# Kernel tuning notes

Hardware: AMD Instinct MI355X
Metric: run time of the kernel (lower is better)

## Reference

```python
import jax, jax.numpy as jnp
import numpy as np

HEADS, D_K = 8, 64   # dim=512 -> d_k = dim//heads = 64; with dim_head=64 the rearrange collapses to [B,H,N,d_k]
EPS = 1e-5


def _per_head_layernorm(t, g, b):
    # t: [B,H,N,D]; g,b: [H,D] (independent LayerNorm per head, biased variance like torch)
    mu = t.mean(-1, keepdims=True)
    var = ((t - mu) ** 2).mean(-1, keepdims=True)
    return (t - mu) * jax.lax.rsqrt(var + EPS) * g[None, :, None, :] + b[None, :, None, :]


def setup_inputs() -> dict:
    key = jax.random.key(0)
    k0, k1, k2, k3, k4, k5 = jax.random.split(key, 6)
    B, N, DIM = 4, 2048, 512
    inner = HEADS * D_K  # = DIM here
    x = jax.random.normal(k0, (B, N, DIM), jnp.float32)
    W_qkv = jax.random.normal(k1, (DIM, 3 * inner), jnp.float32) * (DIM ** -0.5)  # xavier-ish, no bias
    g_q = 1.0 + 0.1 * jax.random.normal(k2, (HEADS, D_K), jnp.float32)
    b_q = 0.1 * jax.random.normal(k3, (HEADS, D_K), jnp.float32)
    g_k = 1.0 + 0.1 * jax.random.normal(k4, (HEADS, D_K), jnp.float32)
    b_k = 0.1 * jax.random.normal(k5, (HEADS, D_K), jnp.float32)
    return {"x": x, "W_qkv": W_qkv, "g_q": g_q, "b_q": b_q, "g_k": g_k, "b_k": b_k}


def reference(x, W_qkv, g_q, b_q, g_k, b_k):
    B, N, _ = x.shape
    qkv = x @ W_qkv                              # [B,N,3*H*D]
    q, k, v = jnp.split(qkv, 3, axis=-1)

    def split_heads(t):
        return t.reshape(B, N, HEADS, D_K).transpose(0, 2, 1, 3)  # [B,H,N,D]

    q, k, v = map(split_heads, (q, k, v))
    q = _per_head_layernorm(q, g_q, b_q)
    k = _per_head_layernorm(k, g_k, b_k)
    # un-normalized linear attention: scale by 1/sqrt(d_k) then by 1/seq_len (no softmax)
    dots = jnp.einsum('bhnd,bhmd->bhnm', q, k) * (D_K ** -0.5)
    p_attn = dots / N
    out = jnp.einsum('bhnm,bhmd->bhnd', p_attn, v)  # [B,H,N,D]
    return out.transpose(0, 2, 1, 3).reshape(B, N, HEADS * D_K)
```

## Files before the change

kernel.cpp:

```cpp
#include <hip/hip_runtime.h>
#include <hip/hip_bf16.h>
#include <stdint.h>

using bf16   = __bf16;
using bf16x4 = __attribute__((ext_vector_type(4))) __bf16;
using bf16x8 = __attribute__((ext_vector_type(8))) __bf16;
using f32x4  = __attribute__((ext_vector_type(4))) float;

static constexpr int BATCH = 4, SEQ = 2048, DIM = 512, HEADS = 8, DK = 64;
static constexpr int M    = BATCH * SEQ;
static constexpr int NQKV = 3 * DIM;

#define GLD16(src, dst)                                                        \
    __builtin_amdgcn_global_load_lds(                                          \
        (const __attribute__((address_space(1))) void*)(src),                  \
        (__attribute__((address_space(3))) void*)(dst), 16, 0, 0)

__global__ __launch_bounds__(256) void k_prep(const float* __restrict__ x,
                                              const float* __restrict__ w,
                                              bf16* __restrict__ xbf,
                                              bf16* __restrict__ wt,
                                              float* __restrict__ S)
{
    const int bid = blockIdx.x;
    const int t   = threadIdx.x;
    const int XB  = (M * DIM) / (256 * 4);
    const int WB  = (DIM / 32) * (NQKV / 32);

    if (bid < XB) {
        const int i = (bid * 256 + t) * 4;
        float4 v = *(const float4*)(x + i);
        bf16x4 o = { (bf16)v.x, (bf16)v.y, (bf16)v.z, (bf16)v.w };
        *(bf16x4*)(xbf + i) = o;
    } else if (bid < XB + WB) {
        const int wb = bid - XB;
        const int rt = wb / 48, ct = wb - rt * 48;
        __shared__ float tile[32][33];
        const int r = t >> 5, c = t & 31;
        #pragma unroll
        for (int i = 0; i < 4; ++i)
            tile[r + i * 8][c] = w[(rt * 32 + r + i * 8) * NQKV + ct * 32 + c];
        __syncthreads();
        #pragma unroll
        for (int i = 0; i < 4; ++i)
            wt[(ct * 32 + r + i * 8) * DIM + rt * 32 + c] = (bf16)tile[c][r + i * 8];
    } else {
        const int sb = bid - XB - WB;
        const int i  = (sb * 256 + t) * 4;
        *(f32x4*)(S + i) = (f32x4){0.f, 0.f, 0.f, 0.f};
    }
}

__global__ __launch_bounds__(384) void k_gemm(const bf16* __restrict__ xbf,
                                              const bf16* __restrict__ Wt,
                                              const float* __restrict__ gq,
                                              const float* __restrict__ bq,
                                              const float* __restrict__ gk,
                                              const float* __restrict__ bk,
                                              bf16* __restrict__ qn,
                                              float* __restrict__ S)
{
    __shared__ union {
        struct { bf16 A[2][128 * 64]; bf16 B[2][192 * 64]; } g;
        struct { bf16 q[2][64][72]; bf16 kst[64 * 128]; bf16 vst[64 * 128]; } e;
    } u;

    const int t    = threadIdx.x;
    const int lane = t & 63, wave = t >> 6;
    const int wm   = wave & 1, ws = wave >> 1;
    const int orig = blockIdx.x;
    const int wg   = (orig & 7) * 64 + (orig >> 3);
    const int mt   = wg >> 3, h = wg & 7;
    const int m0   = mt * 128;

    const int l15 = lane & 15, l4 = lane >> 4;
    const int rl  = lane >> 3, cl = (lane & 7) ^ rl;

    auto stage = [&](int buf, int k0) {
        for (int c = wave; c < 40; c += 6) {
            if (c < 16) {
                const int r = c * 8 + rl;
                GLD16(xbf + (m0 + r) * 512 + k0 + cl * 8, u.g.A[buf] + c * 512);
            } else {
                const int ch  = c - 16;
                const int sec = ch >> 3;
                const int r   = (ch & 7) * 8 + rl;
                GLD16(Wt + ((sec * 512 + h * 64 + r) * 512 + k0 + cl * 8),
                      u.g.B[buf] + ch * 512);
            }
        }
    };

    f32x4 acc[4][4] = {};

    stage(0, 0);
    __syncthreads();
    int cur = 0;
    for (int it = 0; it < 8; ++it) {
        if (it < 7) stage(cur ^ 1, (it + 1) * 64);
        #pragma unroll
        for (int kh = 0; kh < 2; ++kh) {
            bf16x8 af[4], bfv[4];
            const int rc = kh * 4 + l4;
            #pragma unroll
            for (int mf = 0; mf < 4; ++mf) {
                const int row = wm * 64 + mf * 16 + l15;
                af[mf] = *(const bf16x8*)(u.g.A[cur] + row * 64 + ((rc ^ (row & 7)) * 8));
            }
            #pragma unroll
            for (int nf = 0; nf < 4; ++nf) {
                const int row = ws * 64 + nf * 16 + l15;
                bfv[nf] = *(const bf16x8*)(u.g.B[cur] + row * 64 + ((rc ^ (row & 7)) * 8));
            }
            #pragma unroll
            for (int mf = 0; mf < 4; ++mf)
                #pragma unroll
                for (int nf = 0; nf < 4; ++nf)
                    acc[mf][nf] = __builtin_amdgcn_mfma_f32_16x16x32_bf16(
                        af[mf], bfv[nf], acc[mf][nf], 0, 0, 0);
        }
        __syncthreads();
        cur ^= 1;
    }

    const int b  = m0 >> 11;
    const int bh = b * 8 + h;
    const int nwbase = (m0 & 2047) + wm * 64;

    if (ws < 2) {
        const float* gp = (ws == 0 ? gq : gk) + h * 64;
        const float* bp = (ws == 0 ? bq : bk) + h * 64;
        float gv[4], bv[4];
        #pragma unroll
        for (int nf = 0; nf < 4; ++nf) {
            gv[nf] = gp[nf * 16 + l15];
            bv[nf] = bp[nf * 16 + l15];
        }
        #pragma unroll
        for (int mf = 0; mf < 4; ++mf) {
            float mu[4], rs[4];
            #pragma unroll
            for (int r = 0; r < 4; ++r) {
                float s = 0.f, s2 = 0.f;
                #pragma unroll
                for (int nf = 0; nf < 4; ++nf) {
                    const float xv = acc[mf][nf][r];
                    s += xv; s2 += xv * xv;
                }
                s  += __shfl_xor(s, 1);  s  += __shfl_xor(s, 2);
                s  += __shfl_xor(s, 4);  s  += __shfl_xor(s, 8);
                s2 += __shfl_xor(s2, 1); s2 += __shfl_xor(s2, 2);
                s2 += __shfl_xor(s2, 4); s2 += __shfl_xor(s2, 8);
                mu[r] = s * (1.f / 64.f);
                rs[r] = rsqrtf(s2 * (1.f / 64.f) - mu[r] * mu[r] + 1e-5f);
            }
            #pragma unroll
            for (int nf = 0; nf < 4; ++nf) {
                bf16x4 pk;
                #pragma unroll
                for (int r = 0; r < 4; ++r)
                    pk[r] = (bf16)((acc[mf][nf][r] - mu[r]) * rs[r] * gv[nf] + bv[nf]);
                if (ws == 0) {
                    *(bf16x4*)(&u.e.q[wm][nf * 16 + l15][mf * 16 + l4 * 4]) = pk;
                } else {
                    const int d = nf * 16 + l15;
                    const int c = wm * 8 + mf * 2 + (l4 >> 1);
                    *(bf16x4*)(u.e.kst + d * 128 + ((c ^ (d & 7)) * 8) + (l4 & 1) * 4) = pk;
                }
            }
        }
    } else {
        #pragma unroll
        for (int mf = 0; mf < 4; ++mf)
            #pragma unroll
            for (int nf = 0; nf < 4; ++nf) {
                bf16x4 pk;
                #pragma unroll
                for (int r = 0; r < 4; ++r) pk[r] = (bf16)acc[mf][nf][r];
                const int d = nf * 16 + l15;
                const int c = wm * 8 + mf * 2 + (l4 >> 1);
                *(bf16x4*)(u.e.vst + d * 128 + ((c ^ (d & 7)) * 8) + (l4 & 1) * 4) = pk;
            }
    }

    if (ws == 0) {
        bf16* dst = qn + ((long)bh * SEQ + nwbase) * 64;
        const int nq = lane & 15, dq2 = lane >> 4;
        #pragma unroll
        for (int j = 0; j < 4; ++j) {
            const int d0 = (j * 4 + dq2) * 4;
            bf16x4 a0 = *(const bf16x4*)(&u.e.q[wm][d0 + 0][nq * 4]);
            bf16x4 a1 = *(const bf16x4*)(&u.e.q[wm][d0 + 1][nq * 4]);
            bf16x4 a2 = *(const bf16x4*)(&u.e.q[wm][d0 + 2][nq * 4]);
            bf16x4 a3 = *(const bf16x4*)(&u.e.q[wm][d0 + 3][nq * 4]);
            #pragma unroll
            for (int c = 0; c < 4; ++c) {
                bf16x4 o = { a0[c], a1[c], a2[c], a3[c] };
                *(bf16x4*)(dst + (nq * 4 + c) * 64 + d0) = o;
            }
        }
    }

    __syncthreads();

    if (ws == 2) {
        f32x4 sac[4][4] = {};
        #pragma unroll
        for (int kk = 0; kk < 2; ++kk) {
            const int ksi = wm * 2 + kk;
            const int c   = ksi * 4 + l4;
            bf16x8 av[4], bk8[4];
            #pragma unroll
            for (int i = 0; i < 4; ++i) {
                const int dp = i * 16 + l15;
                av[i] = *(const bf16x8*)(u.e.vst + dp * 128 + ((c ^ (dp & 7)) * 8));
            }
            #pragma unroll
            for (int j = 0; j < 4; ++j) {
                const int dd = j * 16 + l15;
                bk8[j] = *(const bf16x8*)(u.e.kst + dd * 128 + ((c ^ (dd & 7)) * 8));
            }
            #pragma unroll
            for (int i = 0; i < 4; ++i)
                #pragma unroll
                for (int j = 0; j < 4; ++j)
                    sac[i][j] = __builtin_amdgcn_mfma_f32_16x16x32_bf16(
                        av[i], bk8[j], sac[i][j], 0, 0, 0);
        }
        float* Sb = S + bh * 4096;
        #pragma unroll
        for (int i = 0; i < 4; ++i)
            #pragma unroll
            for (int j = 0; j < 4; ++j)
                #pragma unroll
                for (int r = 0; r < 4; ++r) {
                    const int dp = i * 16 + l4 * 4 + r;
                    const int dd = j * 16 + l15;
                    atomicAdd(Sb + dp * 64 + dd, sac[i][j][r]);
                }
    }
}

__global__ __launch_bounds__(256) void k_out(const bf16* __restrict__ qn,
                                             const float* __restrict__ S,
                                             float* __restrict__ out)
{
    const int bid = blockIdx.x;
    const int bh = bid >> 4, nt4 = bid & 15;
    const int b = bh >> 3, h = bh & 7;
    const int t = threadIdx.x, lane = t & 63, wave = t >> 6;
    const int l15 = lane & 15, l4 = lane >> 4;
    const float* Sb = S + bh * 4096;
    const float scale = 1.f / 16384.f;

    bf16x8 bfr[2][4];
    #pragma unroll
    for (int kh = 0; kh < 2; ++kh)
        #pragma unroll
        for (int cf = 0; cf < 4; ++cf) {
            const float* p = Sb + (cf * 16 + l15) * 64 + kh * 32 + l4 * 8;
            float4 lo = *(const float4*)(p);
            float4 hi = *(const float4*)(p + 4);
            bf16x8 f;
            f[0] = (bf16)(lo.x * scale); f[1] = (bf16)(lo.y * scale);
            f[2] = (bf16)(lo.z * scale); f[3] = (bf16)(lo.w * scale);
            f[4] = (bf16)(hi.x * scale); f[5] = (bf16)(hi.y * scale);
            f[6] = (bf16)(hi.z * scale); f[7] = (bf16)(hi.w * scale);
            bfr[kh][cf] = f;
        }

    const bf16* qb = qn + (long)bh * SEQ * 64;
    const int nbase = nt4 * 128 + wave * 32;

    #pragma unroll
    for (int mf = 0; mf < 2; ++mf) {
        bf16x8 a0 = *(const bf16x8*)(qb + (nbase + mf * 16 + l15) * 64 +      l4 * 8);
        bf16x8 a1 = *(const bf16x8*)(qb + (nbase + mf * 16 + l15) * 64 + 32 + l4 * 8);
        f32x4 acc[4] = {};
        #pragma unroll
        for (int cf = 0; cf < 4; ++cf) {
            acc[cf] = __builtin_amdgcn_mfma_f32_16x16x32_bf16(a0, bfr[0][cf], acc[cf], 0, 0, 0);
            acc[cf] = __builtin_amdgcn_mfma_f32_16x16x32_bf16(a1, bfr[1][cf], acc[cf], 0, 0, 0);
        }
        #pragma unroll
        for (int cf = 0; cf < 4; ++cf)
            #pragma unroll
            for (int r = 0; r < 4; ++r) {
                const int n = nbase + mf * 16 + l4 * 4 + r;
                out[((long)b * SEQ + n) * 512 + h * 64 + cf * 16 + l15] = acc[cf][r];
            }
    }
}

extern "C" void kernel_launch(void* const* d_in, const int* in_sizes, int n_in,
                              void* d_out, int out_size, void* d_ws, size_t ws_size,
                              hipStream_t stream)
{
    const float* x  = (const float*)d_in[0];
    const float* w  = (const float*)d_in[1];
    const float* gq = (const float*)d_in[2];
    const float* bq = (const float*)d_in[3];
    const float* gk = (const float*)d_in[4];
    const float* bk = (const float*)d_in[5];
    float* out = (float*)d_out;

    char* ws = (char*)d_ws;
    bf16*  xbf = (bf16*)(ws);
    bf16*  wt  = (bf16*)(ws + 8388608);
    bf16*  qn  = (bf16*)(ws + 9961472);
    float* S   = (float*)(ws + 18350080);

    hipLaunchKernelGGL(k_prep, dim3(4096 + 768 + 128), dim3(256), 0, stream,
                       x, w, xbf, wt, S);
    hipLaunchKernelGGL(k_gemm, dim3(512), dim3(384), 0, stream,
                       xbf, wt, gq, bq, gk, bk, qn, S);
    hipLaunchKernelGGL(k_out,  dim3(512), dim3(256), 0, stream, qn, S, out);
}
```

Baseline: 129.3 us.

## Triple-buffer GEMM K-loop with 32-wide slices and explicit vmcnt waits

```diff
diff --git a/kernel.cpp b/kernel.cpp
--- a/kernel.cpp
+++ b/kernel.cpp
@@ -15,6 +15,9 @@
     __builtin_amdgcn_global_load_lds(                                          \
         (const __attribute__((address_space(1))) void*)(src),                  \
         (__attribute__((address_space(3))) void*)(dst), 16, 0, 0)
+
+#define WAITVM(N)  asm volatile("s_waitcnt vmcnt(" #N ")" ::: "memory")
+#define WAITLGKM0  asm volatile("s_waitcnt lgkmcnt(0)" ::: "memory")
 
 __global__ __launch_bounds__(256) void k_prep(const float* __restrict__ x,
                                               const float* __restrict__ w,
@@ -61,7 +64,7 @@
                                               float* __restrict__ S)
 {
     __shared__ union {
-        struct { bf16 A[2][128 * 64]; bf16 B[2][192 * 64]; } g;
+        struct { bf16 A[3][128 * 32]; bf16 B[3][192 * 32]; } g;
         struct { bf16 q[2][64][72]; bf16 kst[64 * 128]; bf16 vst[64 * 128]; } e;
     } u;
 
@@ -74,54 +77,68 @@
     const int m0   = mt * 128;
 
     const int l15 = lane & 15, l4 = lane >> 4;
-    const int rl  = lane >> 3, cl = (lane & 7) ^ rl;
-
-    auto stage = [&](int buf, int k0) {
-        for (int c = wave; c < 40; c += 6) {
-            if (c < 16) {
-                const int r = c * 8 + rl;
-                GLD16(xbf + (m0 + r) * 512 + k0 + cl * 8, u.g.A[buf] + c * 512);
+    const int r4l = lane >> 2, c4 = lane & 3;
+
+    auto stage = [&](int sl, int k0) {
+        for (int c = wave; c < 20; c += 6) {
+            if (c < 8) {
+                const int r = c * 16 + r4l;
+                GLD16(xbf + (m0 + r) * 512 + k0 + ((c4 ^ (r & 3)) * 8),
+                      u.g.A[sl] + c * 512);
             } else {
-                const int ch  = c - 16;
-                const int sec = ch >> 3;
-                const int r   = (ch & 7) * 8 + rl;
-                GLD16(Wt + ((sec * 512 + h * 64 + r) * 512 + k0 + cl * 8),
-                      u.g.B[buf] + ch * 512);
+                const int rb  = (c - 8) * 16 + r4l;
+                const int sec = rb >> 6, rin = rb & 63;
+                GLD16(Wt + ((sec * 512 + h * 64 + rin) * 512 + k0 + ((c4 ^ (rb & 3)) * 8)),
+                      u.g.B[sl] + (c - 8) * 512);
             }
         }
     };
 
     f32x4 acc[4][4] = {};
 
+    auto compute = [&](int sl) {
+        bf16x8 af[4], bfv[4];
+        #pragma unroll
+        for (int mf = 0; mf < 4; ++mf) {
+            const int row = wm * 64 + mf * 16 + l15;
+            af[mf] = *(const bf16x8*)(u.g.A[sl] + row * 32 + ((l4 ^ (row & 3)) * 8));
+        }
+        #pragma unroll
+        for (int nf = 0; nf < 4; ++nf) {
+            const int row = ws * 64 + nf * 16 + l15;
+            bfv[nf] = *(const bf16x8*)(u.g.B[sl] + row * 32 + ((l4 ^ (row & 3)) * 8));
+        }
+        #pragma unroll
+        for (int mf = 0; mf < 4; ++mf)
+            #pragma unroll
+            for (int nf = 0; nf < 4; ++nf)
+                acc[mf][nf] = __builtin_amdgcn_mfma_f32_16x16x32_bf16(
+                    af[mf], bfv[nf], acc[mf][nf], 0, 0, 0);
+    };
+
     stage(0, 0);
-    __syncthreads();
-    int cur = 0;
-    for (int it = 0; it < 8; ++it) {
-        if (it < 7) stage(cur ^ 1, (it + 1) * 64);
-        #pragma unroll
-        for (int kh = 0; kh < 2; ++kh) {
-            bf16x8 af[4], bfv[4];
-            const int rc = kh * 4 + l4;
-            #pragma unroll
-            for (int mf = 0; mf < 4; ++mf) {
-                const int row = wm * 64 + mf * 16 + l15;
-                af[mf] = *(const bf16x8*)(u.g.A[cur] + row * 64 + ((rc ^ (row & 7)) * 8));
-            }
-            #pragma unroll
-            for (int nf = 0; nf < 4; ++nf) {
-                const int row = ws * 64 + nf * 16 + l15;
-                bfv[nf] = *(const bf16x8*)(u.g.B[cur] + row * 64 + ((rc ^ (row & 7)) * 8));
-            }
-            #pragma unroll
-            for (int mf = 0; mf < 4; ++mf)
-                #pragma unroll
-                for (int nf = 0; nf < 4; ++nf)
-                    acc[mf][nf] = __builtin_amdgcn_mfma_f32_16x16x32_bf16(
-                        af[mf], bfv[nf], acc[mf][nf], 0, 0, 0);
-        }
-        __syncthreads();
-        cur ^= 1;
-    }
+    stage(1, 32);
+
+#define GEMM_STEP(T, WA, WB_)                                                  \
+    {                                                                          \
+        if ((T) < 14) stage(((T) + 2) % 3, ((T) + 2) * 32);                    \
+        if (wave < 2) { WAITVM(WA); } else { WAITVM(WB_); }                    \
+        __builtin_amdgcn_sched_barrier(0);                                     \
+        __builtin_amdgcn_s_barrier();            \
+        compute((T) % 3);                                                      \
+        WAITLGKM0;                                       \
+        __builtin_amdgcn_sched_barrier(0);                                     \
+        __builtin_amdgcn_s_barrier();               \
+    }
+
+    GEMM_STEP(0, 8, 6);  GEMM_STEP(1, 8, 6);  GEMM_STEP(2, 8, 6);
+    GEMM_STEP(3, 8, 6);  GEMM_STEP(4, 8, 6);  GEMM_STEP(5, 8, 6);
+    GEMM_STEP(6, 8, 6);  GEMM_STEP(7, 8, 6);  GEMM_STEP(8, 8, 6);
+    GEMM_STEP(9, 8, 6);  GEMM_STEP(10, 8, 6); GEMM_STEP(11, 8, 6);
+    GEMM_STEP(12, 8, 6); GEMM_STEP(13, 8, 6);
+    GEMM_STEP(14, 4, 3);
+    GEMM_STEP(15, 0, 0);
+#undef GEMM_STEP
 
     const int b  = m0 >> 11;
     const int bh = b * 8 + h;
```

Measured after the change: 135.4 us. 1.05x slower.
